# Kernel optimization log

Hardware: AMD Instinct MI355X
Metric: run time of the kernel (lower is better)

## Reference

```python
import jax, jax.numpy as jnp
import numpy as np

B, OBS, H, OUT, T = 4096, 256, 1024, 256, 20


def setup_inputs() -> dict:
    key = jax.random.key(0)
    ks = jax.random.split(key, 10)
    def w(k, shape, fan_in, scale=1.0):
        return (jax.random.normal(k, shape, jnp.float32) / np.sqrt(fan_in)) * scale
    return {
        "x": jax.random.normal(ks[0], (B, OBS), jnp.float32),
        "h": jax.random.normal(ks[1], (B, H), jnp.float32) * 0.1,
        "c": jax.random.normal(ks[2], (B, H), jnp.float32) * 0.1,
        "t": jnp.arange(T, dtype=jnp.float32) * 0.05,  # sorted time grid, total span ~1
        "W_i2h": w(ks[3], (OBS + H, H), OBS + H),
        "b_i2h": jnp.zeros((H,), jnp.float32),
        "W_h2o": w(ks[4], (H, OUT), H),
        "b_h2o": jnp.zeros((OUT,), jnp.float32),
        "Wf1": w(ks[5], (H, H), H),
        "bf1": jnp.zeros((H,), jnp.float32),
        "Wf2": w(ks[6], (H, H), H, scale=0.1),  # keep ODE dynamics mild
        "bf2": jnp.zeros((H,), jnp.float32),
    }


def _odeint_rk4(f, h0, t):
    # Fixed-step RK4 through the given time grid; returns solution at t[-1]
    dts = jnp.diff(t)
    def step(h, dt):
        k1 = f(h)
        k2 = f(h + 0.5 * dt * k1)
        k3 = f(h + 0.5 * dt * k2)
        k4 = f(h + dt * k3)
        return h + (dt / 6.0) * (k1 + 2.0 * k2 + 2.0 * k3 + k4), None
    hT, _ = jax.lax.scan(step, h0, dts)
    return hT


def reference(x, h, c, t, W_i2h, b_i2h, W_h2o, b_h2o, Wf1, bf1, Wf2, bf2):
    # ODE RHS: Linear -> tanh -> Linear (autonomous)
    func = lambda hh: jnp.tanh(hh @ Wf1 + bf1) @ Wf2 + bf2
    # i, f, o gates are identical in the original (same Linear on same 'combined'):
    gate = jax.nn.sigmoid(jnp.concatenate([x, h], axis=-1) @ W_i2h + b_i2h)
    h_ode = _odeint_rk4(func, h, t)
    c_tilde = jax.nn.sigmoid(jnp.concatenate([x, h_ode], axis=-1) @ W_i2h + b_i2h)
    c_new = gate * c + gate * c_tilde  # f*c + i*c_tilde with f == i == gate
    h_new = gate * jnp.tanh(c_new)     # o == gate
    out = h_new @ W_h2o + b_h2o
    return out, h_new, c_new
```

## Files before the change

### kernel.cpp

```cpp
#include <hip/hip_runtime.h>
#include <stdint.h>
#include <math.h>


typedef __attribute__((ext_vector_type(8))) short short8;
typedef __attribute__((ext_vector_type(4))) float float4v;

#define BK 64

__device__ __forceinline__ float bf2f(unsigned short u) {
  union { unsigned int i; float f; } x;
  x.i = ((unsigned int)u) << 16;
  return x.f;
}
__device__ __forceinline__ unsigned short f2bf(float f) {
  union { float f; unsigned int i; } x;
  x.f = f;
  unsigned int r = x.i + 0x7fffu + ((x.i >> 16) & 1u);
  return (unsigned short)(r >> 16);
}
__device__ __forceinline__ void load16(const void* g, void* l) {
  __builtin_amdgcn_global_load_lds(
      (__attribute__((address_space(1))) void*)g,
      (__attribute__((address_space(3))) void*)l, 16, 0, 0);
}
__device__ __forceinline__ short8 packbf8(const float* p) {
  float4v lo = *(const float4v*)p, hi = *(const float4v*)(p + 4);
  short8 s;
  s[0] = (short)f2bf(lo[0]); s[1] = (short)f2bf(lo[1]);
  s[2] = (short)f2bf(lo[2]); s[3] = (short)f2bf(lo[3]);
  s[4] = (short)f2bf(hi[0]); s[5] = (short)f2bf(hi[1]);
  s[6] = (short)f2bf(hi[2]); s[7] = (short)f2bf(hi[3]);
  return s;
}
__device__ __forceinline__ float vsub_uniform(float a, float b) {
  float av;
  asm("v_mov_b32 %0, %1" : "=v"(av) : "s"(a));
  return av - b;
}

template <int MODE, int ADT>
__global__ __launch_bounds__(256, 4) void gemm_ode(
    const void* Av, const unsigned short* __restrict__ Bt,
    int N, int K,
    const float* __restrict__ bias, const float* __restrict__ tgrid,
    int step, int first,
    unsigned short* __restrict__ u1b,
    unsigned short* __restrict__ Tb,
    unsigned short* __restrict__ Sb,
    unsigned short* __restrict__ t1dst,
    const void* aux,
    const float* __restrict__ c2,
    float* __restrict__ outF) {
  __shared__ short8 AsV[2][512];
  __shared__ short8 BsV[2][512];

  const int t = threadIdx.x;
  int bx = blockIdx.x, by = blockIdx.y;
  if (gridDim.x == 16 && gridDim.y == 64) {
    const int lin = bx + (by << 4);
    const int x = lin & 7, j = lin >> 3;
    bx = j & 15;
    by = (x << 3) | (j >> 4);
  }
  const int mBase = by * 64, nBase = bx * 64;
  const int wave = t >> 6, lane = t & 63;
  const int wr = wave >> 1, wc = wave & 1;
  const int q = lane >> 4, m16 = lane & 15;

  float4v acc[2][2];
#pragma unroll
  for (int r = 0; r < 2; ++r)
#pragma unroll
    for (int c = 0; c < 2; ++c) acc[r][c] = (float4v){0.f, 0.f, 0.f, 0.f};

  const int r0 = t >> 3;
  const int kcl = (t & 7) ^ (r0 & 7);
  const unsigned short* aU = (const unsigned short*)Av + (size_t)(mBase + r0) * K + kcl * 8;
  const float* aF = (const float*)Av + (size_t)(mBase + r0) * K + kcl * 8;
  const unsigned short* bG = Bt + (size_t)(nBase + r0) * K + kcl * 8;

  auto computeT = [&](int buf) {
#pragma unroll
    for (int kk = 0; kk < 2; ++kk) {
      const int kc = kk * 4 + q;
      short8 af[2], bfr[2];
#pragma unroll
      for (int r = 0; r < 2; ++r) {
        const int arow = wr * 32 + r * 16 + m16;
        af[r] = AsV[buf][arow * 8 + (kc ^ (arow & 7))];
        const int brow = wc * 32 + r * 16 + m16;
        bfr[r] = BsV[buf][brow * 8 + (kc ^ (brow & 7))];
      }
#pragma unroll
      for (int r = 0; r < 2; ++r)
#pragma unroll
        for (int c = 0; c < 2; ++c)
          acc[r][c] = __builtin_amdgcn_mfma_f32_16x16x32_bf16(af[r], bfr[c],
                                                              acc[r][c], 0, 0, 0);
    }
  };

  if constexpr (ADT == 1) {
    auto stageT = [&](int buf, int k0) {
      load16(aU + k0, &AsV[buf][t]);
      load16(aU + (size_t)32 * K + k0, &AsV[buf][t + 256]);
      load16(bG + k0, &BsV[buf][t]);
      load16(bG + (size_t)32 * K + k0, &BsV[buf][t + 256]);
    };
    stageT(0, 0);
    int cur = 0;
    for (int k0 = BK; k0 < K; k0 += BK) {
      stageT(cur ^ 1, k0);
      asm volatile("s_waitcnt vmcnt(4)" ::: "memory");
      __builtin_amdgcn_sched_barrier(0);
      __builtin_amdgcn_s_barrier();
      __builtin_amdgcn_sched_barrier(0);
      computeT(cur);
      asm volatile("s_waitcnt lgkmcnt(0)" ::: "memory");
      __builtin_amdgcn_sched_barrier(0);
      __builtin_amdgcn_s_barrier();
      __builtin_amdgcn_sched_barrier(0);
      cur ^= 1;
    }
    asm volatile("s_waitcnt vmcnt(0)" ::: "memory");
    __builtin_amdgcn_sched_barrier(0);
    __builtin_amdgcn_s_barrier();
    __builtin_amdgcn_sched_barrier(0);
    computeT(cur);
  } else {
    for (int k0 = 0; k0 < K; k0 += BK) {
      AsV[0][t] = packbf8(aF + k0);
      AsV[0][t + 256] = packbf8(aF + (size_t)32 * K + k0);
      load16(bG + k0, &BsV[0][t]);
      load16(bG + (size_t)32 * K + k0, &BsV[0][t + 256]);
      __builtin_amdgcn_s_waitcnt(0);
      __syncthreads();
      computeT(0);
      __syncthreads();
    }
  }

  float dtv = 0.f;
  if constexpr (MODE >= 1 && MODE <= 4) dtv = vsub_uniform(tgrid[step + 1], tgrid[step]);
  if constexpr (MODE == 5) dtv = vsub_uniform(tgrid[step], tgrid[0]);

  const int colBase = nBase + wc * 32 + m16;
  const int rowBase = mBase + wr * 32 + q * 4;
#pragma unroll
  for (int r = 0; r < 2; ++r) {
#pragma unroll
    for (int c = 0; c < 2; ++c) {
      const int col = colBase + c * 16;
#pragma unroll
      for (int e = 0; e < 4; ++e) {
        const int row = rowBase + r * 16 + e;
        const size_t idx = (size_t)row * N + col;
        const float v = acc[r][c][e];
        if constexpr (MODE == 0) {
          const float u1 = v + bias[col];
          u1b[idx] = f2bf(u1);
          t1dst[idx] = f2bf(tanhf(u1));
        } else if constexpr (MODE == 1) {
          const float u2 = bf2f(u1b[idx]) + 0.5f * dtv * (v + c2[col]);
          const float th = tanhf(u2);
          t1dst[idx] = f2bf(th);
          Tb[idx] = f2bf(bf2f(((const unsigned short*)aux)[idx]) + 2.f * th);
        } else if constexpr (MODE == 2) {
          const float u3 = bf2f(u1b[idx]) + 0.5f * dtv * (v + c2[col]);
          const float th = tanhf(u3);
          t1dst[idx] = f2bf(th);
          Tb[idx] = f2bf(bf2f(Tb[idx]) + 2.f * th);
        } else if constexpr (MODE == 3) {
          const float u4 = bf2f(u1b[idx]) + dtv * (v + c2[col]);
          Tb[idx] = f2bf(bf2f(Tb[idx]) + tanhf(u4));
        } else if constexpr (MODE == 4) {
          const float u1n = bf2f(u1b[idx]) + (dtv * (1.f / 6.f)) * v + dtv * c2[col];
          u1b[idx] = f2bf(u1n);
          t1dst[idx] = f2bf(tanhf(u1n));
          const float sOld = first ? 0.f : bf2f(Sb[idx]);
          Sb[idx] = f2bf(sOld + (dtv * (1.f / 6.f)) *
                                    bf2f(((const unsigned short*)aux)[idx]));
        } else if constexpr (MODE == 5) {
          const float z = ((const float*)aux)[idx] + v + dtv * bias[col];
          t1dst[idx] = f2bf(z);
        } else if constexpr (MODE == 6) {
          t1dst[(size_t)col * 1024 + row] = f2bf(v);
        } else {
          outF[idx] = v + bias[col];
        }
      }
    }
  }
}

__global__ __launch_bounds__(256, 4) void gemm_fused(
    const float* __restrict__ x, const float* __restrict__ h,
    const unsigned short* __restrict__ zB,
    const unsigned short* __restrict__ WiT,
    const float* __restrict__ bi, const float* __restrict__ c_in,
    float* __restrict__ hnewF, float* __restrict__ cnewF) {
  __shared__ short8 AsG[512];
  __shared__ short8 AsC[512];
  __shared__ short8 Bs[512];

  const int t = threadIdx.x;
  int bx = blockIdx.x, by = blockIdx.y;
  if (gridDim.x == 16 && gridDim.y == 64) {
    const int lin = bx + (by << 4);
    const int xc = lin & 7, j = lin >> 3;
    bx = j & 15;
    by = (xc << 3) | (j >> 4);
  }
  const int mBase = by * 64, nBase = bx * 64;
  const int wave = t >> 6, lane = t & 63;
  const int wr = wave >> 1, wc = wave & 1;
  const int q = lane >> 4, m16 = lane & 15;

  float4v accG[2][2], accC[2][2];
#pragma unroll
  for (int r = 0; r < 2; ++r)
#pragma unroll
    for (int c = 0; c < 2; ++c) {
      accG[r][c] = (float4v){0.f, 0.f, 0.f, 0.f};
      accC[r][c] = (float4v){0.f, 0.f, 0.f, 0.f};
    }

  const int r0 = t >> 3;
  const int kcl = (t & 7) ^ (r0 & 7);

  for (int k0 = 0; k0 < 1280; k0 += BK) {
    const bool isX = (k0 < 256);
#pragma unroll
    for (int i = 0; i < 2; ++i) {
      const int row = mBase + r0 + i * 32;
      short8 sg, sc;
      if (isX) {
        sg = packbf8(x + (size_t)row * 256 + k0 + kcl * 8);
        sc = sg;
      } else {
        const size_t off = (size_t)row * 1024 + (k0 - 256) + kcl * 8;
        sg = packbf8(h + off);
        sc = *(const short8*)(zB + off);
      }
      AsG[i * 256 + t] = sg;
      AsC[i * 256 + t] = sc;
      load16(WiT + (size_t)(nBase + r0 + i * 32) * 1280 + k0 + kcl * 8,
             &Bs[i * 256 + t]);
    }
    __builtin_amdgcn_s_waitcnt(0);
    __syncthreads();

#pragma unroll
    for (int kk = 0; kk < 2; ++kk) {
      const int kc = kk * 4 + q;
      short8 ag[2], ac[2], bfr[2];
#pragma unroll
      for (int r = 0; r < 2; ++r) {
        const int arow = wr * 32 + r * 16 + m16;
        ag[r] = AsG[arow * 8 + (kc ^ (arow & 7))];
        ac[r] = AsC[arow * 8 + (kc ^ (arow & 7))];
        const int brow = wc * 32 + r * 16 + m16;
        bfr[r] = Bs[brow * 8 + (kc ^ (brow & 7))];
      }
#pragma unroll
      for (int r = 0; r < 2; ++r)
#pragma unroll
        for (int c = 0; c < 2; ++c) {
          accG[r][c] = __builtin_amdgcn_mfma_f32_16x16x32_bf16(ag[r], bfr[c],
                                                               accG[r][c], 0, 0, 0);
          accC[r][c] = __builtin_amdgcn_mfma_f32_16x16x32_bf16(ac[r], bfr[c],
                                                               accC[r][c], 0, 0, 0);
        }
    }
    __syncthreads();
  }

  const int colBase = nBase + wc * 32 + m16;
  const int rowBase = mBase + wr * 32 + q * 4;
#pragma unroll
  for (int r = 0; r < 2; ++r) {
#pragma unroll
    for (int c = 0; c < 2; ++c) {
      const int col = colBase + c * 16;
      const float bv = bi[col];
#pragma unroll
      for (int e = 0; e < 4; ++e) {
        const int row = rowBase + r * 16 + e;
        const size_t idx = (size_t)row * 1024 + col;
        const float g = 1.f / (1.f + expf(-(accG[r][c][e] + bv)));
        const float ct = 1.f / (1.f + expf(-(accC[r][c][e] + bv)));
        const float cn = g * (c_in[idx] + ct);
        const float hn = g * tanhf(cn);
        hnewF[idx] = hn;
        cnewF[idx] = cn;
      }
    }
  }
}

__global__ __launch_bounds__(256) void transpose_f32_bf16(
    const float* __restrict__ in, unsigned short* __restrict__ out,
    int R, int C) {
  __shared__ float tile[32][33];
  const int c0 = blockIdx.x * 32, r0 = blockIdx.y * 32;
  const int tx = threadIdx.x, ty = threadIdx.y;
#pragma unroll
  for (int i = 0; i < 32; i += 8)
    tile[ty + i][tx] = in[(size_t)(r0 + ty + i) * C + c0 + tx];
  __syncthreads();
#pragma unroll
  for (int i = 0; i < 32; i += 8)
    out[(size_t)(c0 + ty + i) * R + r0 + tx] = f2bf(tile[tx][ty + i]);
}

__global__ __launch_bounds__(256) void c2_gemv(
    const float* __restrict__ b2, const float* __restrict__ W1,
    float* __restrict__ c2v) {
  const int n = blockIdx.x * 256 + threadIdx.x;
  float a = 0.f;
  for (int k = 0; k < 1024; ++k) a += b2[k] * W1[(size_t)k * 1024 + n];
  c2v[n] = a;
}

extern "C" void kernel_launch(void* const* d_in, const int* in_sizes, int n_in,
                              void* d_out, int out_size, void* d_ws, size_t ws_size,
                              hipStream_t stream) {
  const float* x  = (const float*)d_in[0];
  const float* h  = (const float*)d_in[1];
  const float* c  = (const float*)d_in[2];
  const float* t  = (const float*)d_in[3];
  const float* Wi = (const float*)d_in[4];
  const float* bi = (const float*)d_in[5];
  const float* Wo = (const float*)d_in[6];
  const float* bo = (const float*)d_in[7];
  const float* W1 = (const float*)d_in[8];
  const float* b1 = (const float*)d_in[9];
  const float* W2 = (const float*)d_in[10];
  const float* b2 = (const float*)d_in[11];

  const size_t MB = 1ull << 20;
  char* ws = (char*)d_ws;
  unsigned short* W21T = (unsigned short*)(ws);
  unsigned short* W2T  = (unsigned short*)(ws + 2 * MB);
  unsigned short* WiT  = (unsigned short*)(ws + 4 * MB);
  unsigned short* WoT  = (unsigned short*)(ws + 6 * MB + 512 * 1024);
  unsigned short* P0   = (unsigned short*)(ws + 7 * MB);

  float*          outF  = (float*)d_out;
  float*          hnewF = outF + 1048576;
  float*          cnewF = outF + 5242880;
  unsigned short* u1b   = (unsigned short*)d_out;
  unsigned short* Tb    = (unsigned short*)((char*)d_out + 8 * MB);
  unsigned short* P1    = (unsigned short*)((char*)d_out + 16 * MB);
  unsigned short* Sb    = (unsigned short*)((char*)d_out + 24 * MB);
  unsigned short* W1T   = (unsigned short*)((char*)d_out + 32 * MB);
  float*          c2v   = (float*)((char*)d_out + 34 * MB);

  const dim3 tb(32, 8), blk(256), g(16, 64);

  transpose_f32_bf16<<<dim3(32, 32), tb, 0, stream>>>(W1, W1T, 1024, 1024);
  transpose_f32_bf16<<<dim3(32, 32), tb, 0, stream>>>(W2, W2T, 1024, 1024);
  transpose_f32_bf16<<<dim3(32, 40), tb, 0, stream>>>(Wi, WiT, 1280, 1024);
  transpose_f32_bf16<<<dim3(8, 32),  tb, 0, stream>>>(Wo, WoT, 1024, 256);
  c2_gemv<<<4, blk, 0, stream>>>(b2, W1, c2v);
  gemm_ode<6, 0><<<dim3(16, 16), blk, 0, stream>>>(
      W2, W1T, 1024, 1024, b1, t, 0, 0,
      nullptr, nullptr, nullptr, W21T, nullptr, nullptr, nullptr);
  gemm_ode<0, 0><<<g, blk, 0, stream>>>(
      h, W1T, 1024, 1024, b1, t, 0, 0,
      u1b, nullptr, nullptr, P0, nullptr, nullptr, nullptr);

  for (int s = 0; s < 19; ++s) {
    gemm_ode<1, 1><<<g, blk, 0, stream>>>(
        P0, W21T, 1024, 1024, b1, t, s, 0,
        u1b, Tb, nullptr, P1, P0, c2v, nullptr);
    gemm_ode<2, 1><<<g, blk, 0, stream>>>(
        P1, W21T, 1024, 1024, b1, t, s, 0,
        u1b, Tb, nullptr, P0, nullptr, c2v, nullptr);
    gemm_ode<3, 1><<<g, blk, 0, stream>>>(
        P0, W21T, 1024, 1024, b1, t, s, 0,
        u1b, Tb, nullptr, nullptr, nullptr, c2v, nullptr);
    gemm_ode<4, 1><<<g, blk, 0, stream>>>(
        Tb, W21T, 1024, 1024, b1, t, s, (s == 0) ? 1 : 0,
        u1b, nullptr, Sb, P0, Tb, c2v, nullptr);
  }

  gemm_ode<5, 1><<<g, blk, 0, stream>>>(
      Sb, W2T, 1024, 1024, b2, t, 19, 0,
      nullptr, nullptr, nullptr, P0, h, nullptr, nullptr);

  gemm_fused<<<g, blk, 0, stream>>>(x, h, P0, WiT, bi, c, hnewF, cnewF);

  gemm_ode<7, 0><<<dim3(4, 64), blk, 0, stream>>>(
      hnewF, WoT, 256, 1024, bo, t, 0, 0,
      nullptr, nullptr, nullptr, nullptr, nullptr, nullptr, outF);
}
```

Measured before the change: 1.736 ms.

## Software-pipeline gemm_fused loads with register prefetch and double-buffered B tile

Restructures the fused gate GEMM main loop so the global loads for the next K-tile (A operands into registers and the B tile into a second LDS buffer) are issued before the current tile is converted, stored and computed. Explicit vmcnt waits and sched barriers are meant to hide global memory latency behind the MFMA work. In exchange it uses more registers and LDS, which may lower occupancy. It also makes the block swizzle unconditional, which assumes a 16x64 grid. The x path issues extra redundant short8 loads so the vmcnt count stays uniform.

```diff
diff --git a/kernel.cpp b/kernel.cpp
--- a/kernel.cpp
+++ b/kernel.cpp
@@ -26,6 +26,14 @@
 }
 __device__ __forceinline__ short8 packbf8(const float* p) {
   float4v lo = *(const float4v*)p, hi = *(const float4v*)(p + 4);
+  short8 s;
+  s[0] = (short)f2bf(lo[0]); s[1] = (short)f2bf(lo[1]);
+  s[2] = (short)f2bf(lo[2]); s[3] = (short)f2bf(lo[3]);
+  s[4] = (short)f2bf(hi[0]); s[5] = (short)f2bf(hi[1]);
+  s[6] = (short)f2bf(hi[2]); s[7] = (short)f2bf(hi[3]);
+  return s;
+}
+__device__ __forceinline__ short8 pack2(float4v lo, float4v hi) {
   short8 s;
   s[0] = (short)f2bf(lo[0]); s[1] = (short)f2bf(lo[1]);
   s[2] = (short)f2bf(lo[2]); s[3] = (short)f2bf(lo[3]);
@@ -202,11 +210,11 @@
     float* __restrict__ hnewF, float* __restrict__ cnewF) {
   __shared__ short8 AsG[512];
   __shared__ short8 AsC[512];
-  __shared__ short8 Bs[512];
+  __shared__ short8 Bs[2][512];
 
   const int t = threadIdx.x;
   int bx = blockIdx.x, by = blockIdx.y;
-  if (gridDim.x == 16 && gridDim.y == 64) {
+  {
     const int lin = bx + (by << 4);
     const int xc = lin & 7, j = lin >> 3;
     bx = j & 15;
@@ -228,29 +236,36 @@
 
   const int r0 = t >> 3;
   const int kcl = (t & 7) ^ (r0 & 7);
-
-  for (int k0 = 0; k0 < 1280; k0 += BK) {
-    const bool isX = (k0 < 256);
-#pragma unroll
-    for (int i = 0; i < 2; ++i) {
-      const int row = mBase + r0 + i * 32;
-      short8 sg, sc;
-      if (isX) {
-        sg = packbf8(x + (size_t)row * 256 + k0 + kcl * 8);
-        sc = sg;
-      } else {
-        const size_t off = (size_t)row * 1024 + (k0 - 256) + kcl * 8;
-        sg = packbf8(h + off);
-        sc = *(const short8*)(zB + off);
-      }
-      AsG[i * 256 + t] = sg;
-      AsC[i * 256 + t] = sc;
-      load16(WiT + (size_t)(nBase + r0 + i * 32) * 1280 + k0 + kcl * 8,
-             &Bs[i * 256 + t]);
-    }
-    __builtin_amdgcn_s_waitcnt(0);
-    __syncthreads();
-
+  const int row0 = mBase + r0, row1 = row0 + 32;
+
+  struct Regs { float4v a0, a1, a2, a3; short8 z0, z1; };
+  Regs Ra, Rb;
+
+  auto issueA = [&](int i, Regs& R) {
+    const int k0 = i * 64;
+    if (k0 < 256) {
+      const float* g0 = x + (size_t)row0 * 256 + k0 + kcl * 8;
+      const float* g1 = x + (size_t)row1 * 256 + k0 + kcl * 8;
+      R.a0 = *(const float4v*)g0; R.a1 = *(const float4v*)(g0 + 4);
+      R.a2 = *(const float4v*)g1; R.a3 = *(const float4v*)(g1 + 4);
+      R.z0 = *(const short8*)(const void*)g0;
+      R.z1 = *(const short8*)(const void*)g1;
+    } else {
+      const size_t o0 = (size_t)row0 * 1024 + (k0 - 256) + kcl * 8;
+      const size_t o1 = (size_t)row1 * 1024 + (k0 - 256) + kcl * 8;
+      R.a0 = *(const float4v*)(h + o0); R.a1 = *(const float4v*)(h + o0 + 4);
+      R.a2 = *(const float4v*)(h + o1); R.a3 = *(const float4v*)(h + o1 + 4);
+      R.z0 = *(const short8*)(zB + o0);
+      R.z1 = *(const short8*)(zB + o1);
+    }
+  };
+  auto issueB = [&](int i, int buf) {
+    const int k0 = i * 64;
+    load16(WiT + (size_t)(nBase + r0) * 1280 + k0 + kcl * 8, &Bs[buf][t]);
+    load16(WiT + (size_t)(nBase + r0 + 32) * 1280 + k0 + kcl * 8,
+           &Bs[buf][t + 256]);
+  };
+  auto computeF = [&](int buf) {
 #pragma unroll
     for (int kk = 0; kk < 2; ++kk) {
       const int kc = kk * 4 + q;
@@ -261,7 +276,7 @@
         ag[r] = AsG[arow * 8 + (kc ^ (arow & 7))];
         ac[r] = AsC[arow * 8 + (kc ^ (arow & 7))];
         const int brow = wc * 32 + r * 16 + m16;
-        bfr[r] = Bs[brow * 8 + (kc ^ (brow & 7))];
+        bfr[r] = Bs[buf][brow * 8 + (kc ^ (brow & 7))];
       }
 #pragma unroll
       for (int r = 0; r < 2; ++r)
@@ -273,7 +288,45 @@
                                                                accC[r][c], 0, 0, 0);
         }
     }
-    __syncthreads();
+  };
+
+  int buf = 0;
+  auto stepF = [&](int i, Regs& Rc, Regs& Rn) {
+    if (i + 1 < 20) {
+      issueA(i + 1, Rn);
+      issueB(i + 1, buf ^ 1);
+      asm volatile("s_waitcnt vmcnt(8)" ::: "memory");
+    } else {
+      asm volatile("s_waitcnt vmcnt(0)" ::: "memory");
+    }
+    __builtin_amdgcn_sched_barrier(0);
+    {
+      const bool isX = (i * 64) < 256;
+      const short8 s0 = pack2(Rc.a0, Rc.a1);
+      const short8 s1 = pack2(Rc.a2, Rc.a3);
+      AsG[t] = s0;
+      AsG[t + 256] = s1;
+      AsC[t] = isX ? s0 : Rc.z0;
+      AsC[t + 256] = isX ? s1 : Rc.z1;
+    }
+    asm volatile("s_waitcnt lgkmcnt(0)" ::: "memory");
+    __builtin_amdgcn_sched_barrier(0);
+    __builtin_amdgcn_s_barrier();
+    __builtin_amdgcn_sched_barrier(0);
+    computeF(buf);
+    asm volatile("s_waitcnt lgkmcnt(0)" ::: "memory");
+    __builtin_amdgcn_sched_barrier(0);
+    __builtin_amdgcn_s_barrier();
+    __builtin_amdgcn_sched_barrier(0);
+    buf ^= 1;
+  };
+
+  issueA(0, Ra);
+  issueB(0, 0);
+#pragma unroll 1
+  for (int ii = 0; ii < 20; ii += 2) {
+    stepF(ii, Ra, Rb);
+    stepF(ii + 1, Rb, Ra);
   }
 
   const int colBase = nBase + wc * 32 + m16;
```

Measured after the change: 1.730 ms. About the same (-0.4%).
